# Kernel optimization log

Measured on AMD Instinct MI355X. Metric: run time of the kernel, lower is better.

Reference implementation:

```python
import jax, jax.numpy as jnp
import numpy as np
import math

N_NODES = 50000
N_EDGES = 800000
F_IN = 32
HID = 64


def _layernorm(x, g, b, eps=1e-5):
    mu = x.mean(-1, keepdims=True)
    var = ((x - mu) ** 2).mean(-1, keepdims=True)
    return (x - mu) / jnp.sqrt(var + eps) * g + b


def _tconv(x, src, dst, Wq, bq, Wk, bk, Wv, bv, Ws, heads):
    # PyG TransformerConv (concat=True, root_weight=True, bias=False on skip)
    N = x.shape[0]
    C = Wq.shape[1] // heads
    q = (x @ Wq + bq).reshape(N, heads, C)[dst]  # [E,H,C] gathered at targets
    k = (x @ Wk + bk).reshape(N, heads, C)[src]  # [E,H,C] gathered at sources
    v = (x @ Wv + bv).reshape(N, heads, C)[src]
    scores = (q * k).sum(-1) / math.sqrt(C)      # [E,H]
    m = jax.ops.segment_max(scores, dst, num_segments=N)   # [N,H]
    p = jnp.exp(scores - m[dst])
    denom = jax.ops.segment_sum(p, dst, num_segments=N)
    alpha = p / (denom[dst] + 1e-16)             # segment softmax over in-edges
    agg = jax.ops.segment_sum(v * alpha[..., None], dst, num_segments=N)
    return agg.reshape(N, heads * C) + x @ Ws    # + skip (no bias)


def setup_inputs() -> dict:
    key = jax.random.key(0)
    ks = iter(jax.random.split(key, 64))
    def rn(shape, s=0.1):
        return jax.random.normal(next(ks), shape, jnp.float32) * s
    inp = {
        "x": rn((N_NODES, F_IN), 1.0),
        "edge_index": jax.random.randint(next(ks), (2, N_EDGES), 0, N_NODES, dtype=jnp.int32),
        "ln0_g": jnp.ones((F_IN,), jnp.float32),
        "ln0_b": jnp.zeros((F_IN,), jnp.float32),
    }
    dims = [F_IN, HID, HID]
    for l in range(3):
        d = dims[l]
        inp[f"Wq{l}"] = rn((d, HID)); inp[f"bq{l}"] = rn((HID,), 0.05)
        inp[f"Wk{l}"] = rn((d, HID)); inp[f"bk{l}"] = rn((HID,), 0.05)
        inp[f"Wv{l}"] = rn((d, HID)); inp[f"bv{l}"] = rn((HID,), 0.05)
        inp[f"Ws{l}"] = rn((d, HID))
        inp[f"g{l}"] = jnp.ones((HID,), jnp.float32)
        inp[f"b{l}"] = jnp.zeros((HID,), jnp.float32)
    inp["Wr1"] = rn((HID, HID // 2)); inp["br1"] = jnp.zeros((HID // 2,), jnp.float32)
    inp["Wr2"] = rn((HID // 2, 1));   inp["br2"] = jnp.zeros((1,), jnp.float32)
    inp["Wt1"] = rn((HID, HID // 2)); inp["bt1"] = jnp.zeros((HID // 2,), jnp.float32)
    inp["Wt2"] = rn((HID // 2, 1));   inp["bt2"] = jnp.zeros((1,), jnp.float32)
    return inp


def reference(x, edge_index, ln0_g, ln0_b,
              Wq0, bq0, Wk0, bk0, Wv0, bv0, Ws0, g0, b0,
              Wq1, bq1, Wk1, bk1, Wv1, bv1, Ws1, g1, b1,
              Wq2, bq2, Wk2, bk2, Wv2, bv2, Ws2, g2, b2,
              Wr1, br1, Wr2, br2, Wt1, bt1, Wt2, bt2):
    src, dst = edge_index[0], edge_index[1]
    h = _layernorm(x, ln0_g, ln0_b)
    layers = [
        (Wq0, bq0, Wk0, bk0, Wv0, bv0, Ws0, g0, b0, 4),
        (Wq1, bq1, Wk1, bk1, Wv1, bv1, Ws1, g1, b1, 4),
        (Wq2, bq2, Wk2, bk2, Wv2, bv2, Ws2, g2, b2, 1),
    ]
    for i, (Wq, bq, Wk, bk, Wv, bv, Ws, g, b, heads) in enumerate(layers):
        x_res = h if h.shape[-1] == HID else None
        h = _tconv(h, src, dst, Wq, bq, Wk, bk, Wv, bv, Ws, heads)
        h = _layernorm(h, g, b)
        if x_res is not None and i > 0:
            h = h + 0.1 * x_res
        if i < len(layers) - 1:
            h = jax.nn.relu(h)  # dropout is identity in eval mode
    rtt = jax.nn.relu(h @ Wr1 + br1) @ Wr2 + br2      # [N,1]
    retrans = jax.nn.relu(h @ Wt1 + bt1) @ Wt2 + bt2  # [N,1]
    return jnp.concatenate([rtt, retrans], axis=1)    # [N,2]
```

## Files before the change

kernel.cpp:

```cpp
#include <hip/hip_runtime.h>
#include <hip/hip_bf16.h>
#include <math.h>

#define N_NODES 50000
#define N_EDGES 800000
#define HID 64
#define NBK 196
#define EPB 1024
#define SB  782
#define FLAT (NBK * SB)
#define SCAN_B ((FLAT + 255) / 256)

typedef __attribute__((ext_vector_type(8))) short short8;
typedef __attribute__((ext_vector_type(4))) float float4v;

__device__ __forceinline__ unsigned short f32_to_bf16_rne(float f) {
    unsigned int u = __float_as_uint(f);
    unsigned int r = u + 0x7fffu + ((u >> 16) & 1u);
    return (unsigned short)(r >> 16);
}

__global__ void ln0_kernel(const float* __restrict__ x,
                           const float* __restrict__ g,
                           const float* __restrict__ b,
                           float* __restrict__ h0) {
    int lane = threadIdx.x & 63;
    int n = blockIdx.x * 8 + (threadIdx.x >> 6) * 2 + (lane >> 5);
    int c = lane & 31;
    float v = x[n * 32 + c];
    float s = v;
    #pragma unroll
    for (int off = 1; off < 32; off <<= 1) s += __shfl_xor(s, off);
    float mu = s * (1.0f / 32.0f);
    float d = v - mu;
    float vs = d * d;
    #pragma unroll
    for (int off = 1; off < 32; off <<= 1) vs += __shfl_xor(vs, off);
    float var = vs * (1.0f / 32.0f);
    float y = d * rsqrtf(var + 1e-5f) * g[c] + b[c];
    h0[n * 32 + c] = y;
}

__global__ __launch_bounds__(256) void hist_kernel(const int* __restrict__ dst,
                                                   int* __restrict__ ghist) {
    __shared__ int hist[NBK];
    int t = threadIdx.x, i = blockIdx.x;
    for (int k = t; k < NBK; k += 256) hist[k] = 0;
    __syncthreads();
    int e0 = i * EPB;
    #pragma unroll
    for (int r = 0; r < 4; r++) {
        int e = e0 + r * 256 + t;
        if (e < N_EDGES) atomicAdd(&hist[dst[e] >> 8], 1);
    }
    __syncthreads();
    for (int k = t; k < NBK; k += 256) ghist[k * SB + i] = hist[k];
}

__global__ void scan1_kernel(const int* __restrict__ ghist, int* __restrict__ csum) {
    int f = blockIdx.x * 256 + threadIdx.x;
    int v = (f < FLAT) ? ghist[f] : 0;
    #pragma unroll
    for (int off = 1; off < 64; off <<= 1) v += __shfl_xor(v, off);
    __shared__ int ws[4];
    if ((threadIdx.x & 63) == 0) ws[threadIdx.x >> 6] = v;
    __syncthreads();
    if (threadIdx.x == 0) csum[blockIdx.x] = ws[0] + ws[1] + ws[2] + ws[3];
}

__global__ void scan2_kernel(const int* __restrict__ csum, int* __restrict__ coff,
                             int* __restrict__ bbase, int* __restrict__ row_ptr) {
    int lane = threadIdx.x;
    int carry = 0;
    for (int base = 0; base < SCAN_B; base += 64) {
        int i = base + lane;
        int v = (i < SCAN_B) ? csum[i] : 0;
        int incl = v;
        #pragma unroll
        for (int off = 1; off < 64; off <<= 1) {
            int tt = __shfl_up(incl, off);
            if (lane >= off) incl += tt;
        }
        if (i < SCAN_B) coff[i] = carry + incl - v;
        carry += __shfl(incl, 63);
    }
    if (lane == 0) { bbase[NBK] = N_EDGES; row_ptr[N_NODES] = N_EDGES; }
}

__global__ void scan3_kernel(const int* __restrict__ ghist, const int* __restrict__ coff,
                             int* __restrict__ goff, int* __restrict__ bbase) {
    int f = blockIdx.x * 256 + threadIdx.x;
    int lane = threadIdx.x & 63;
    int w = threadIdx.x >> 6;
    int v = (f < FLAT) ? ghist[f] : 0;
    int incl = v;
    #pragma unroll
    for (int off = 1; off < 64; off <<= 1) {
        int tt = __shfl_up(incl, off);
        if (lane >= off) incl += tt;
    }
    __shared__ int ws[4];
    if (lane == 63) ws[w] = incl;
    __syncthreads();
    int woff = 0;
    #pragma unroll
    for (int k = 0; k < 4; k++) if (k < w) woff += ws[k];
    int excl = coff[blockIdx.x] + woff + incl - v;
    if (f < FLAT) {
        goff[f] = excl;
        if (f % SB == 0) bbase[f / SB] = excl;
    }
}

__global__ __launch_bounds__(256) void scatter_kernel(
        const int* __restrict__ src, const int* __restrict__ dst,
        const int* __restrict__ goff, int2* __restrict__ ebkt) {
    __shared__ int hist[NBK];
    int t = threadIdx.x, i = blockIdx.x;
    for (int k = t; k < NBK; k += 256) hist[k] = 0;
    __syncthreads();
    int e0 = i * EPB;
    #pragma unroll
    for (int r = 0; r < 4; r++) {
        int e = e0 + r * 256 + t;
        if (e < N_EDGES) {
            int s = src[e], d = dst[e];
            int k = d >> 8;
            int rank = atomicAdd(&hist[k], 1);
            ebkt[goff[k * SB + i] + rank] = make_int2(s, d);
        }
    }
}

__global__ __launch_bounds__(256) void bucket_build_kernel(
        const int2* __restrict__ ebkt, const int* __restrict__ bbase,
        int* __restrict__ row_ptr, int* __restrict__ colb) {
    __shared__ int ldeg[256];
    __shared__ int lcur[256];
    __shared__ int wsum[4];
    int b = blockIdx.x;
    int t = threadIdx.x;
    int cbase = bbase[b];
    int cnt = bbase[b + 1] - cbase;
    int ebase = cbase;

    ldeg[t] = 0;
    __syncthreads();
    for (int i = t; i < cnt; i += 256) {
        int2 e = ebkt[ebase + i];
        atomicAdd(&ldeg[e.y & 255], 1);
    }
    __syncthreads();

    int lane = t & 63;
    int w = t >> 6;
    int v = ldeg[t];
    int incl = v;
    #pragma unroll
    for (int off = 1; off < 64; off <<= 1) {
        int tt = __shfl_up(incl, off);
        if (lane >= off) incl += tt;
    }
    if (lane == 63) wsum[w] = incl;
    __syncthreads();
    int woff = 0;
    #pragma unroll
    for (int k = 0; k < 4; k++) if (k < w) woff += wsum[k];
    int excl = woff + incl - v;

    int node = b * 256 + t;
    if (node < N_NODES) row_ptr[node] = cbase + excl;
    lcur[t] = excl;
    __syncthreads();

    for (int i = t; i < cnt; i += 256) {
        int2 e = ebkt[ebase + i];
        int r = atomicAdd(&lcur[e.y & 255], 1);
        colb[cbase + r] = e.x;
    }
}

__global__ void wprep_kernel(const float* __restrict__ Wq, const float* __restrict__ Wk,
                             const float* __restrict__ Wv, const float* __restrict__ Ws,
                             int KS, unsigned short* __restrict__ Wp) {
    int idx = blockIdx.x * 256 + threadIdx.x;
    int total = 16 * KS * 512;
    if (idx >= total) return;
    int j = idx & 7;
    int lane = (idx >> 3) & 63;
    int ts = idx >> 9;
    int s = ts % KS;
    int tile = ts / KS;
    int which = tile >> 2;
    int slice = tile & 3;
    int k = s * 32 + ((lane >> 4) * 8) + j;
    int col = slice * 16 + (lane & 15);
    const float* W = (which == 0) ? Wq : (which == 1) ? Wk : (which == 2) ? Wv : Ws;
    Wp[idx] = f32_to_bf16_rne(W[k * 64 + col]);
}

template <int D>
__global__ __launch_bounds__(256) void qkvs_mfma_kernel(
        const float* __restrict__ h,
        const unsigned short* __restrict__ Wp,
        const float* __restrict__ bq, const float* __restrict__ bk,
        const float* __restrict__ bv,
        float* __restrict__ Q, unsigned int* __restrict__ KV,
        float* __restrict__ S) {
    constexpr int KS = D / 32;
    int t = threadIdx.x;
    int lane = t & 63;
    int w = t >> 6;
    int n0 = blockIdx.x * 16;
    int n16 = lane & 15;
    int quad = lane >> 4;
    int col = w * 16 + n16;

    short8 afrag[KS];
    #pragma unroll
    for (int s = 0; s < KS; s++) {
        const float* hp = &h[(n0 + n16) * D + s * 32 + quad * 8];
        float4 a0 = *(const float4*)hp;
        float4 a1 = *(const float4*)(hp + 4);
        short8 af;
        af[0] = (short)f32_to_bf16_rne(a0.x);
        af[1] = (short)f32_to_bf16_rne(a0.y);
        af[2] = (short)f32_to_bf16_rne(a0.z);
        af[3] = (short)f32_to_bf16_rne(a0.w);
        af[4] = (short)f32_to_bf16_rne(a1.x);
        af[5] = (short)f32_to_bf16_rne(a1.y);
        af[6] = (short)f32_to_bf16_rne(a1.z);
        af[7] = (short)f32_to_bf16_rne(a1.w);
        afrag[s] = af;
    }

    float4v accs[4];
    #pragma unroll
    for (int which = 0; which < 4; which++) {
        float4v acc = {0.0f, 0.0f, 0.0f, 0.0f};
        int tile = which * 4 + w;
        #pragma unroll
        for (int s = 0; s < KS; s++) {
            short8 bfrag = *(const short8*)&Wp[((tile * KS + s) * 64 + lane) * 8];
            acc = __builtin_amdgcn_mfma_f32_16x16x32_bf16(afrag[s], bfrag, acc, 0, 0, 0);
        }
        accs[which] = acc;
    }

    float bqc = bq[col], bkc = bk[col], bvc = bv[col];

    #pragma unroll
    for (int r = 0; r < 4; r++) {
        int node = n0 + quad * 4 + r;
        Q[node * 64 + col] = accs[0][r] + bqc;
        unsigned int kw = f32_to_bf16_rne(accs[1][r] + bkc);
        unsigned int vw = f32_to_bf16_rne(accs[2][r] + bvc);
        KV[node * 64 + col] = (vw << 16) | kw;
        S[node * 64 + col] = accs[3][r];
    }
}

template <int HEADS, bool RES, bool RELU>
__global__ __launch_bounds__(256) void agg_kernel(
                           const float* __restrict__ Q, const unsigned int* __restrict__ KV,
                           const float* __restrict__ S,
                           const int* __restrict__ row_ptr, const int* __restrict__ colb,
                           const float* __restrict__ g, const float* __restrict__ b,
                           const float* __restrict__ h_in, float* __restrict__ h_out) {
    constexpr int C = HID / HEADS;
    int lane = threadIdx.x & 63;
    int m = lane & 15;
    int grp = lane >> 4;
    int n = blockIdx.x * 4 + (threadIdx.x >> 6);

    const float scale = rsqrtf((float)C);
    float4 q4 = *(const float4*)&Q[n * 64 + 4 * m];
    q4.x *= scale; q4.y *= scale; q4.z *= scale; q4.w *= scale;

    int beg = row_ptr[n], end = row_ptr[n + 1];

    float ssum = 0.0f;
    float acc0 = 0.0f, acc1 = 0.0f, acc2 = 0.0f, acc3 = 0.0f;

    for (int base = beg; base < end; base += 64) {
        int limit = end - base;
        int src_l = (base + lane < end) ? colb[base + lane] : 0;
        int iters = (min(limit, 64) + 3) >> 2;
        #pragma unroll 4
        for (int jj = 0; jj < iters; jj++) {
            int esl = jj * 4 + grp;
            int src = __shfl(src_l, esl);
            uint4 kv = *(const uint4*)&KV[src * 64 + 4 * m];
            float k0 = __uint_as_float(kv.x << 16), v0 = __uint_as_float(kv.x & 0xffff0000u);
            float k1 = __uint_as_float(kv.y << 16), v1 = __uint_as_float(kv.y & 0xffff0000u);
            float k2 = __uint_as_float(kv.z << 16), v2 = __uint_as_float(kv.z & 0xffff0000u);
            float k3 = __uint_as_float(kv.w << 16), v3 = __uint_as_float(kv.w & 0xffff0000u);
            float tq = fmaf(q4.x, k0, fmaf(q4.y, k1, fmaf(q4.z, k2, q4.w * k3)));
            #pragma unroll
            for (int off = 1; off < C / 4; off <<= 1) tq += __shfl_xor(tq, off);
            float p = (esl < limit) ? __expf(tq) : 0.0f;
            ssum += p;
            acc0 = fmaf(p, v0, acc0);
            acc1 = fmaf(p, v1, acc1);
            acc2 = fmaf(p, v2, acc2);
            acc3 = fmaf(p, v3, acc3);
        }
    }

    #pragma unroll
    for (int off = 16; off < 64; off <<= 1) {
        ssum += __shfl_xor(ssum, off);
        acc0 += __shfl_xor(acc0, off);
        acc1 += __shfl_xor(acc1, off);
        acc2 += __shfl_xor(acc2, off);
        acc3 += __shfl_xor(acc3, off);
    }

    float inv = 1.0f / (ssum + 1e-16f);
    float4 sv = *(const float4*)&S[n * 64 + 4 * m];
    float o0 = fmaf(acc0, inv, sv.x);
    float o1 = fmaf(acc1, inv, sv.y);
    float o2 = fmaf(acc2, inv, sv.z);
    float o3 = fmaf(acc3, inv, sv.w);

    float s = (o0 + o1) + (o2 + o3);
    #pragma unroll
    for (int off = 1; off < 16; off <<= 1) s += __shfl_xor(s, off);
    float mu = s * (1.0f / 64.0f);
    float d0 = o0 - mu, d1 = o1 - mu, d2 = o2 - mu, d3 = o3 - mu;
    float vs = (d0 * d0 + d1 * d1) + (d2 * d2 + d3 * d3);
    #pragma unroll
    for (int off = 1; off < 16; off <<= 1) vs += __shfl_xor(vs, off);
    float rstd = rsqrtf(vs * (1.0f / 64.0f) + 1e-5f);

    float4 gv = *(const float4*)&g[4 * m];
    float4 bv = *(const float4*)&b[4 * m];
    float y0 = d0 * rstd * gv.x + bv.x;
    float y1 = d1 * rstd * gv.y + bv.y;
    float y2 = d2 * rstd * gv.z + bv.z;
    float y3 = d3 * rstd * gv.w + bv.w;
    if (RES) {
        float4 rv = *(const float4*)&h_in[n * 64 + 4 * m];
        y0 = fmaf(0.1f, rv.x, y0);
        y1 = fmaf(0.1f, rv.y, y1);
        y2 = fmaf(0.1f, rv.z, y2);
        y3 = fmaf(0.1f, rv.w, y3);
    }
    if (RELU) {
        y0 = fmaxf(y0, 0.0f); y1 = fmaxf(y1, 0.0f);
        y2 = fmaxf(y2, 0.0f); y3 = fmaxf(y3, 0.0f);
    }
    if (grp == 0) {
        float4 yv = make_float4(y0, y1, y2, y3);
        *(float4*)&h_out[n * 64 + 4 * m] = yv;
    }
}

__global__ void head_kernel(const float* __restrict__ h,
                            const float* __restrict__ Wr1, const float* __restrict__ br1,
                            const float* __restrict__ Wr2, const float* __restrict__ br2,
                            const float* __restrict__ Wt1, const float* __restrict__ bt1,
                            const float* __restrict__ Wt2, const float* __restrict__ bt2,
                            float* __restrict__ out) {
    __shared__ float sh[4][HID];
    int wave = threadIdx.x >> 6;
    int lane = threadIdx.x & 63;
    int n = blockIdx.x * 4 + wave;
    sh[wave][lane] = h[n * 64 + lane];
    __syncthreads();
    int half = lane >> 5;
    int j = lane & 31;
    const float* W1 = half ? Wt1 : Wr1;
    const float* b1 = half ? bt1 : br1;
    const float* W2 = half ? Wt2 : Wr2;
    const float* b2 = half ? bt2 : br2;
    float a = b1[j];
    #pragma unroll 8
    for (int i = 0; i < 64; i++) a = fmaf(sh[wave][i], W1[i * 32 + j], a);
    a = fmaxf(a, 0.0f);
    float r = a * W2[j];
    #pragma unroll
    for (int off = 1; off < 32; off <<= 1) r += __shfl_xor(r, off);
    if (j == 0) out[n * 2 + half] = r + b2[0];
}

extern "C" void kernel_launch(void* const* d_in, const int* in_sizes, int n_in,
                              void* d_out, int out_size, void* d_ws, size_t ws_size,
                              hipStream_t stream) {
    const float* x    = (const float*)d_in[0];
    const int*   ei   = (const int*)d_in[1];
    const int*   src  = ei;
    const int*   dst  = ei + N_EDGES;
    const float* ln0g = (const float*)d_in[2];
    const float* ln0b = (const float*)d_in[3];

    const float* P[27];
    for (int i = 0; i < 27; i++) P[i] = (const float*)d_in[4 + i];
    const float* Wr1 = (const float*)d_in[31];
    const float* br1 = (const float*)d_in[32];
    const float* Wr2 = (const float*)d_in[33];
    const float* br2 = (const float*)d_in[34];
    const float* Wt1 = (const float*)d_in[35];
    const float* bt1 = (const float*)d_in[36];
    const float* Wt2 = (const float*)d_in[37];
    const float* bt2 = (const float*)d_in[38];

    float* out = (float*)d_out;

    float* hbuf0 = (float*)d_ws;
    float* hbuf1 = hbuf0 + N_NODES * 64;
    float* Qb    = hbuf1 + N_NODES * 64;
    float* Sb    = Qb + N_NODES * 64;
    unsigned int* KVb = (unsigned int*)(Sb + N_NODES * 64);
    int* row_ptr = (int*)(KVb + N_NODES * 64);
    int* colb    = row_ptr + (N_NODES + 1);
    int* ghist   = colb + N_EDGES;
    int* goff    = ghist + FLAT;
    int* csum    = goff + FLAT;
    int* coff    = csum + SCAN_B;
    int* bbase   = coff + SCAN_B;
    unsigned short* Wp0 = (unsigned short*)(bbase + NBK + 1);
    unsigned short* Wp1 = Wp0 + 16 * 1 * 512;
    unsigned short* Wp2 = Wp1 + 16 * 2 * 512;
    int2* ebkt = (int2*)Qb;

    ln0_kernel<<<6250, 256, 0, stream>>>(x, ln0g, ln0b, hbuf0);
    hist_kernel<<<SB, 256, 0, stream>>>(dst, ghist);
    scan1_kernel<<<SCAN_B, 256, 0, stream>>>(ghist, csum);
    scan2_kernel<<<1, 64, 0, stream>>>(csum, coff, bbase, row_ptr);
    scan3_kernel<<<SCAN_B, 256, 0, stream>>>(ghist, coff, goff, bbase);
    scatter_kernel<<<SB, 256, 0, stream>>>(src, dst, goff, ebkt);
    bucket_build_kernel<<<NBK, 256, 0, stream>>>(ebkt, bbase, row_ptr, colb);
    wprep_kernel<<<32, 256, 0, stream>>>(P[0],  P[2],  P[4],  P[6],  1, Wp0);
    wprep_kernel<<<64, 256, 0, stream>>>(P[9],  P[11], P[13], P[15], 2, Wp1);
    wprep_kernel<<<64, 256, 0, stream>>>(P[18], P[20], P[22], P[24], 2, Wp2);

    qkvs_mfma_kernel<32><<<3125, 256, 0, stream>>>(hbuf0, Wp0,
        P[1], P[3], P[5], Qb, KVb, Sb);
    agg_kernel<4, false, true><<<12500, 256, 0, stream>>>(Qb, KVb, Sb,
        row_ptr, colb, P[7], P[8], nullptr, hbuf1);

    qkvs_mfma_kernel<64><<<3125, 256, 0, stream>>>(hbuf1, Wp1,
        P[10], P[12], P[14], Qb, KVb, Sb);
    agg_kernel<4, true, true><<<12500, 256, 0, stream>>>(Qb, KVb, Sb,
        row_ptr, colb, P[16], P[17], hbuf1, hbuf0);

    qkvs_mfma_kernel<64><<<3125, 256, 0, stream>>>(hbuf0, Wp2,
        P[19], P[21], P[23], Qb, KVb, Sb);
    agg_kernel<1, true, false><<<12500, 256, 0, stream>>>(Qb, KVb, Sb,
        row_ptr, colb, P[25], P[26], hbuf0, hbuf1);

    head_kernel<<<12500, 256, 0, stream>>>(hbuf1,
        Wr1, br1, Wr2, br2, Wt1, bt1, Wt2, bt2, out);
}
```

Before: 367.7 us.

## Merge prep kernels into one launch and batch four edge gathers in aggregation

Folds ln0, the dst histogram and the three weight-prep kernels into a single block-dispatched prep kernel, cutting four launches and the serialisation between them. Also restructures the aggregation inner loop to issue four independent KV gathers per step, then do their dot-product reductions and exp/accumulate together. This is meant to raise memory-level parallelism on the latency-bound gather. The cost is higher register pressure and some wasted lanes when the last 16-edge chunk is only partly filled.

```diff
diff --git a/kernel.cpp b/kernel.cpp
--- a/kernel.cpp
+++ b/kernel.cpp
@@ -11,6 +11,12 @@
 #define FLAT (NBK * SB)
 #define SCAN_B ((FLAT + 255) / 256)
 
+#define LN0_BLKS   6250
+#define HIST_BLKS  SB
+#define WP0_BLKS   32
+#define WP12_BLKS  64
+#define PREP_BLKS  (LN0_BLKS + HIST_BLKS + WP0_BLKS + 2 * WP12_BLKS)
+
 typedef __attribute__((ext_vector_type(8))) short short8;
 typedef __attribute__((ext_vector_type(4))) float float4v;
 
@@ -20,12 +26,11 @@
     return (unsigned short)(r >> 16);
 }
 
-__global__ void ln0_kernel(const float* __restrict__ x,
-                           const float* __restrict__ g,
-                           const float* __restrict__ b,
-                           float* __restrict__ h0) {
-    int lane = threadIdx.x & 63;
-    int n = blockIdx.x * 8 + (threadIdx.x >> 6) * 2 + (lane >> 5);
+__device__ __forceinline__ void ln0_body(int b, int t,
+        const float* __restrict__ x, const float* __restrict__ g,
+        const float* __restrict__ bb, float* __restrict__ h0) {
+    int lane = t & 63;
+    int n = b * 8 + (t >> 6) * 2 + (lane >> 5);
     int c = lane & 31;
     float v = x[n * 32 + c];
     float s = v;
@@ -37,24 +42,66 @@
     #pragma unroll
     for (int off = 1; off < 32; off <<= 1) vs += __shfl_xor(vs, off);
     float var = vs * (1.0f / 32.0f);
-    float y = d * rsqrtf(var + 1e-5f) * g[c] + b[c];
-    h0[n * 32 + c] = y;
-}
-
-__global__ __launch_bounds__(256) void hist_kernel(const int* __restrict__ dst,
-                                                   int* __restrict__ ghist) {
+    h0[n * 32 + c] = d * rsqrtf(var + 1e-5f) * g[c] + bb[c];
+}
+
+__device__ __forceinline__ void wprep_body(int idx, int KS,
+        const float* __restrict__ Wq, const float* __restrict__ Wk,
+        const float* __restrict__ Wv, const float* __restrict__ Ws,
+        unsigned short* __restrict__ Wp) {
+    int j = idx & 7;
+    int lane = (idx >> 3) & 63;
+    int ts = idx >> 9;
+    int s = ts % KS;
+    int tile = ts / KS;
+    int which = tile >> 2;
+    int slice = tile & 3;
+    int k = s * 32 + ((lane >> 4) * 8) + j;
+    int col = slice * 16 + (lane & 15);
+    const float* W = (which == 0) ? Wq : (which == 1) ? Wk : (which == 2) ? Wv : Ws;
+    Wp[idx] = f32_to_bf16_rne(W[k * 64 + col]);
+}
+
+__global__ __launch_bounds__(256) void prep_kernel(
+        const float* __restrict__ x, const float* __restrict__ ln0g,
+        const float* __restrict__ ln0b, float* __restrict__ h0,
+        const int* __restrict__ dst, int* __restrict__ ghist,
+        const float* __restrict__ Wq0, const float* __restrict__ Wk0,
+        const float* __restrict__ Wv0, const float* __restrict__ Ws0,
+        unsigned short* __restrict__ Wp0,
+        const float* __restrict__ Wq1, const float* __restrict__ Wk1,
+        const float* __restrict__ Wv1, const float* __restrict__ Ws1,
+        unsigned short* __restrict__ Wp1,
+        const float* __restrict__ Wq2, const float* __restrict__ Wk2,
+        const float* __restrict__ Wv2, const float* __restrict__ Ws2,
+        unsigned short* __restrict__ Wp2) {
     __shared__ int hist[NBK];
-    int t = threadIdx.x, i = blockIdx.x;
-    for (int k = t; k < NBK; k += 256) hist[k] = 0;
-    __syncthreads();
-    int e0 = i * EPB;
-    #pragma unroll
-    for (int r = 0; r < 4; r++) {
-        int e = e0 + r * 256 + t;
-        if (e < N_EDGES) atomicAdd(&hist[dst[e] >> 8], 1);
-    }
-    __syncthreads();
-    for (int k = t; k < NBK; k += 256) ghist[k * SB + i] = hist[k];
+    int b = blockIdx.x;
+    int t = threadIdx.x;
+    if (b < LN0_BLKS) {
+        ln0_body(b, t, x, ln0g, ln0b, h0);
+    } else if (b < LN0_BLKS + HIST_BLKS) {
+        int i = b - LN0_BLKS;
+        for (int k = t; k < NBK; k += 256) hist[k] = 0;
+        __syncthreads();
+        int e0 = i * EPB;
+        #pragma unroll
+        for (int r = 0; r < 4; r++) {
+            int e = e0 + r * 256 + t;
+            if (e < N_EDGES) atomicAdd(&hist[dst[e] >> 8], 1);
+        }
+        __syncthreads();
+        for (int k = t; k < NBK; k += 256) ghist[k * SB + i] = hist[k];
+    } else if (b < LN0_BLKS + HIST_BLKS + WP0_BLKS) {
+        int idx = (b - LN0_BLKS - HIST_BLKS) * 256 + t;
+        wprep_body(idx, 1, Wq0, Wk0, Wv0, Ws0, Wp0);
+    } else if (b < LN0_BLKS + HIST_BLKS + WP0_BLKS + WP12_BLKS) {
+        int idx = (b - LN0_BLKS - HIST_BLKS - WP0_BLKS) * 256 + t;
+        wprep_body(idx, 2, Wq1, Wk1, Wv1, Ws1, Wp1);
+    } else {
+        int idx = (b - LN0_BLKS - HIST_BLKS - WP0_BLKS - WP12_BLKS) * 256 + t;
+        wprep_body(idx, 2, Wq2, Wk2, Wv2, Ws2, Wp2);
+    }
 }
 
 __global__ void scan1_kernel(const int* __restrict__ ghist, int* __restrict__ csum) {
@@ -178,25 +225,6 @@
         int r = atomicAdd(&lcur[e.y & 255], 1);
         colb[cbase + r] = e.x;
     }
-}
-
-__global__ void wprep_kernel(const float* __restrict__ Wq, const float* __restrict__ Wk,
-                             const float* __restrict__ Wv, const float* __restrict__ Ws,
-                             int KS, unsigned short* __restrict__ Wp) {
-    int idx = blockIdx.x * 256 + threadIdx.x;
-    int total = 16 * KS * 512;
-    if (idx >= total) return;
-    int j = idx & 7;
-    int lane = (idx >> 3) & 63;
-    int ts = idx >> 9;
-    int s = ts % KS;
-    int tile = ts / KS;
-    int which = tile >> 2;
-    int slice = tile & 3;
-    int k = s * 32 + ((lane >> 4) * 8) + j;
-    int col = slice * 16 + (lane & 15);
-    const float* W = (which == 0) ? Wq : (which == 1) ? Wk : (which == 2) ? Wv : Ws;
-    Wp[idx] = f32_to_bf16_rne(W[k * 64 + col]);
 }
 
 template <int D>
@@ -283,27 +311,65 @@
     float acc0 = 0.0f, acc1 = 0.0f, acc2 = 0.0f, acc3 = 0.0f;
 
     for (int base = beg; base < end; base += 64) {
-        int limit = end - base;
+        int limit = min(end - base, 64);
         int src_l = (base + lane < end) ? colb[base + lane] : 0;
-        int iters = (min(limit, 64) + 3) >> 2;
-        #pragma unroll 4
-        for (int jj = 0; jj < iters; jj++) {
-            int esl = jj * 4 + grp;
-            int src = __shfl(src_l, esl);
-            uint4 kv = *(const uint4*)&KV[src * 64 + 4 * m];
-            float k0 = __uint_as_float(kv.x << 16), v0 = __uint_as_float(kv.x & 0xffff0000u);
-            float k1 = __uint_as_float(kv.y << 16), v1 = __uint_as_float(kv.y & 0xffff0000u);
-            float k2 = __uint_as_float(kv.z << 16), v2 = __uint_as_float(kv.z & 0xffff0000u);
-            float k3 = __uint_as_float(kv.w << 16), v3 = __uint_as_float(kv.w & 0xffff0000u);
-            float tq = fmaf(q4.x, k0, fmaf(q4.y, k1, fmaf(q4.z, k2, q4.w * k3)));
+        for (int sub = 0; sub < limit; sub += 16) {
+            int e0 = sub + grp, e1 = sub + 4 + grp, e2 = sub + 8 + grp, e3 = sub + 12 + grp;
+            int s0 = __shfl(src_l, e0);
+            int s1 = __shfl(src_l, e1);
+            int s2 = __shfl(src_l, e2);
+            int s3 = __shfl(src_l, e3);
+            bool v0ok = e0 < limit, v1ok = e1 < limit, v2ok = e2 < limit, v3ok = e3 < limit;
+            uint4 kv0 = make_uint4(0, 0, 0, 0), kv1 = kv0, kv2 = kv0, kv3 = kv0;
+            if (v0ok) kv0 = *(const uint4*)&KV[(size_t)s0 * 64 + 4 * m];
+            if (v1ok) kv1 = *(const uint4*)&KV[(size_t)s1 * 64 + 4 * m];
+            if (v2ok) kv2 = *(const uint4*)&KV[(size_t)s2 * 64 + 4 * m];
+            if (v3ok) kv3 = *(const uint4*)&KV[(size_t)s3 * 64 + 4 * m];
+
+            float t0 = fmaf(q4.x, __uint_as_float(kv0.x << 16),
+                       fmaf(q4.y, __uint_as_float(kv0.y << 16),
+                       fmaf(q4.z, __uint_as_float(kv0.z << 16),
+                            q4.w * __uint_as_float(kv0.w << 16))));
+            float t1 = fmaf(q4.x, __uint_as_float(kv1.x << 16),
+                       fmaf(q4.y, __uint_as_float(kv1.y << 16),
+                       fmaf(q4.z, __uint_as_float(kv1.z << 16),
+                            q4.w * __uint_as_float(kv1.w << 16))));
+            float t2 = fmaf(q4.x, __uint_as_float(kv2.x << 16),
+                       fmaf(q4.y, __uint_as_float(kv2.y << 16),
+                       fmaf(q4.z, __uint_as_float(kv2.z << 16),
+                            q4.w * __uint_as_float(kv2.w << 16))));
+            float t3 = fmaf(q4.x, __uint_as_float(kv3.x << 16),
+                       fmaf(q4.y, __uint_as_float(kv3.y << 16),
+                       fmaf(q4.z, __uint_as_float(kv3.z << 16),
+                            q4.w * __uint_as_float(kv3.w << 16))));
             #pragma unroll
-            for (int off = 1; off < C / 4; off <<= 1) tq += __shfl_xor(tq, off);
-            float p = (esl < limit) ? __expf(tq) : 0.0f;
-            ssum += p;
-            acc0 = fmaf(p, v0, acc0);
-            acc1 = fmaf(p, v1, acc1);
-            acc2 = fmaf(p, v2, acc2);
-            acc3 = fmaf(p, v3, acc3);
+            for (int off = 1; off < C / 4; off <<= 1) {
+                t0 += __shfl_xor(t0, off);
+                t1 += __shfl_xor(t1, off);
+                t2 += __shfl_xor(t2, off);
+                t3 += __shfl_xor(t3, off);
+            }
+            float p0 = v0ok ? __expf(t0) : 0.0f;
+            float p1 = v1ok ? __expf(t1) : 0.0f;
+            float p2 = v2ok ? __expf(t2) : 0.0f;
+            float p3 = v3ok ? __expf(t3) : 0.0f;
+            ssum += (p0 + p1) + (p2 + p3);
+            acc0 = fmaf(p0, __uint_as_float(kv0.x & 0xffff0000u),
+                   fmaf(p1, __uint_as_float(kv1.x & 0xffff0000u),
+                   fmaf(p2, __uint_as_float(kv2.x & 0xffff0000u),
+                   fmaf(p3, __uint_as_float(kv3.x & 0xffff0000u), acc0))));
+            acc1 = fmaf(p0, __uint_as_float(kv0.y & 0xffff0000u),
+                   fmaf(p1, __uint_as_float(kv1.y & 0xffff0000u),
+                   fmaf(p2, __uint_as_float(kv2.y & 0xffff0000u),
+                   fmaf(p3, __uint_as_float(kv3.y & 0xffff0000u), acc1))));
+            acc2 = fmaf(p0, __uint_as_float(kv0.z & 0xffff0000u),
+                   fmaf(p1, __uint_as_float(kv1.z & 0xffff0000u),
+                   fmaf(p2, __uint_as_float(kv2.z & 0xffff0000u),
+                   fmaf(p3, __uint_as_float(kv3.z & 0xffff0000u), acc2))));
+            acc3 = fmaf(p0, __uint_as_float(kv0.w & 0xffff0000u),
+                   fmaf(p1, __uint_as_float(kv1.w & 0xffff0000u),
+                   fmaf(p2, __uint_as_float(kv2.w & 0xffff0000u),
+                   fmaf(p3, __uint_as_float(kv3.w & 0xffff0000u), acc3))));
         }
     }
 
@@ -424,16 +490,16 @@
     unsigned short* Wp2 = Wp1 + 16 * 2 * 512;
     int2* ebkt = (int2*)Qb;
 
-    ln0_kernel<<<6250, 256, 0, stream>>>(x, ln0g, ln0b, hbuf0);
-    hist_kernel<<<SB, 256, 0, stream>>>(dst, ghist);
+    prep_kernel<<<PREP_BLKS, 256, 0, stream>>>(x, ln0g, ln0b, hbuf0,
+        dst, ghist,
+        P[0],  P[2],  P[4],  P[6],  Wp0,
+        P[9],  P[11], P[13], P[15], Wp1,
+        P[18], P[20], P[22], P[24], Wp2);
     scan1_kernel<<<SCAN_B, 256, 0, stream>>>(ghist, csum);
     scan2_kernel<<<1, 64, 0, stream>>>(csum, coff, bbase, row_ptr);
     scan3_kernel<<<SCAN_B, 256, 0, stream>>>(ghist, coff, goff, bbase);
     scatter_kernel<<<SB, 256, 0, stream>>>(src, dst, goff, ebkt);
     bucket_build_kernel<<<NBK, 256, 0, stream>>>(ebkt, bbase, row_ptr, colb);
-    wprep_kernel<<<32, 256, 0, stream>>>(P[0],  P[2],  P[4],  P[6],  1, Wp0);
-    wprep_kernel<<<64, 256, 0, stream>>>(P[9],  P[11], P[13], P[15], 2, Wp1);
-    wprep_kernel<<<64, 256, 0, stream>>>(P[18], P[20], P[22], P[24], 2, Wp2);
 
     qkvs_mfma_kernel<32><<<3125, 256, 0, stream>>>(hbuf0, Wp0,
         P[1], P[3], P[5], Qb, KVb, Sb);
```

Result: faster. 349.3 us (-5.0%).
